# Kernel optimization log

Hardware: AMD Instinct MI355X
Metric: run time of the kernel (lower is better)

Reference implementation:

```python
import jax, jax.numpy as jnp
import numpy as np

TAU_PRE = 2.0
TAU_POST = 2.0
KH, KW = 3, 3
B, CIN, H, W = 16, 64, 66, 66
COUT = 128
HOUT, WOUT = H - KH + 1, W - KW + 1  # stride 1, padding 0


def setup_inputs() -> dict:
    key = jax.random.key(0)
    k1, k2, k3, k4, k5 = jax.random.split(key, 5)
    in_spike = jax.random.uniform(k1, (B, CIN, H, W), dtype=jnp.float32)
    out_spike = jax.random.uniform(k2, (B, COUT, HOUT, WOUT), dtype=jnp.float32)
    trace_pre = jax.random.uniform(k3, (B, CIN, H, W), dtype=jnp.float32)
    trace_post = jax.random.uniform(k4, (B, COUT, HOUT, WOUT), dtype=jnp.float32)
    weight = jax.random.normal(k5, (COUT, CIN, KH, KW), dtype=jnp.float32) * 0.05
    return {"in_spike": in_spike, "out_spike": out_spike,
            "trace_pre": trace_pre, "trace_post": trace_post, "weight": weight}


def reference(in_spike, out_spike, trace_pre, trace_post, weight):
    # Trace decay + spike accumulation (faithful to torch: tr - tr/tau + spike)
    tr_pre = trace_pre - trace_pre / TAU_PRE + in_spike    # [B,Cin,H,W]
    tr_post = trace_post - trace_post / TAU_POST + out_spike  # [B,Cout,Hout,Wout]

    rows = []
    for h in range(KH):
        cols = []
        for w in range(KW):
            pre = in_spike[:, :, h:h + HOUT, w:w + WOUT]   # [B,Cin,Hout,Wout]
            trp = tr_pre[:, :, h:h + HOUT, w:w + WOUT]     # [B,Cin,Hout,Wout]
            wk = weight[:, :, h, w]                        # [Cout,Cin]
            # sum over batch and spatial dims of outer products
            s_pre = jnp.einsum('bopq,bipq->oi', tr_post, pre)      # [Cout,Cin]
            s_post = jnp.einsum('bipq,bopq->oi', trp, out_spike)   # [Cout,Cin]
            cols.append(-wk * s_pre + wk * s_post)
        rows.append(jnp.stack(cols, axis=-1))  # [Cout,Cin,KW]
    delta_w = jnp.stack(rows, axis=-2)          # [Cout,Cin,KH,KW]
    return tr_pre, tr_post, delta_w
```

## Files before the change

### kernel.cpp

```cpp
#include <hip/hip_runtime.h>


typedef unsigned short ushort_t;
typedef unsigned int uint_t;
typedef __attribute__((ext_vector_type(8))) short short8;
typedef __attribute__((ext_vector_type(4))) float floatx4;
typedef __attribute__((ext_vector_type(2))) float floatx2;
typedef __attribute__((ext_vector_type(4))) int intx4;
typedef __attribute__((ext_vector_type(2))) unsigned int uintx2;

#define N_PRE   4460544
#define N_POST  8388608
#define N_DW    73728
#define O_TRPOST 4460544
#define O_DW     12849152
#define BROWS   67584
#define BRAW    4866048

#define FILL_A_BLOCKS 1280
#define FILL_B_BLOCKS 768
#define FILL_BLOCKS   2048
#define B_ROWS_PER_WAVE 22

#define GLDS16(g, l) __builtin_amdgcn_global_load_lds( \
    (const __attribute__((address_space(1))) void*)(g), \
    (__attribute__((address_space(3))) void*)(l), 16, 0, 0)

__device__ __forceinline__ ushort_t f2bf(float f) {
  uint_t u = __builtin_bit_cast(uint_t, f);
  u = (u + 0x7FFFu + ((u >> 16) & 1u)) >> 16;
  return (ushort_t)u;
}

__device__ __forceinline__ uint_t pk2bf(float a, float b) {
  return (uint_t)f2bf(a) | ((uint_t)f2bf(b) << 16);
}

__device__ __forceinline__ int bsh2(int hi, int lo) {
  return (int)((((unsigned long long)(uint_t)hi << 32) | (uint_t)lo) >> 16);
}

__global__ __launch_bounds__(256)
void k_fill(const float* __restrict__ in_sp, const float* __restrict__ out_sp,
            const float* __restrict__ tpre, const float* __restrict__ tpost,
            float* __restrict__ o_trpre, float* __restrict__ o_trpost,
            ushort_t* __restrict__ A1, ushort_t* __restrict__ A2,
            ushort_t* __restrict__ B1, ushort_t* __restrict__ B2, int use_ws) {
  const int bx = blockIdx.x;
  if (bx < FILL_A_BLOCKS) {
    const int n4 = N_POST / 4;
    const int stride = FILL_A_BLOCKS * 256;
    for (int i4 = bx * 256 + (int)threadIdx.x; i4 < n4; i4 += stride) {
      floatx4 o = *(const floatx4*)(out_sp + i4 * 4);
      floatx4 p = *(const floatx4*)(tpost + i4 * 4);
      *(floatx4*)(o_trpost + i4 * 4) = 0.5f * p + o;
      if (use_ws) {
        uintx2 va = { pk2bf(o.x, o.y), pk2bf(o.z, o.w) };
        uintx2 vn = { pk2bf(-p.x, -p.y), pk2bf(-p.z, -p.w) };
        *(uintx2*)(A1 + i4 * 4) = va;
        *(uintx2*)(A2 + i4 * 4) = vn;
      }
    }
  } else {
    const int l = threadIdx.x & 63;
    if (l >= 33) return;
    const int wid = (bx - FILL_A_BLOCKS) * 4 + ((int)threadIdx.x >> 6);
    #pragma unroll 2
    for (int it = 0; it < B_ROWS_PER_WAVE; ++it) {
      const int row = wid * B_ROWS_PER_WAVE + it;
      const int g = row * 66 + l * 2;
      floatx2 a = *(const floatx2*)(tpre + g);
      floatx2 c = *(const floatx2*)(in_sp + g);
      floatx2 v = { 0.5f * a.x + c.x, 0.5f * a.y + c.y };
      *(floatx2*)(o_trpre + g) = v;
      if (use_ws) {
        *(uint_t*)(B1 + row * 72 + l * 2) = pk2bf(a.x, a.y);
        *(uint_t*)(B2 + row * 72 + l * 2) = pk2bf(c.x, c.y);
      }
    }
  }
}

__global__ __launch_bounds__(256, 2)
void k_mfma(const ushort_t* __restrict__ A1, const ushort_t* __restrict__ B1,
            float* __restrict__ partials) {
  __shared__ short LA[16384];
  __shared__ short LB[64 * 152];

  const int kh = blockIdx.y, bx = blockIdx.x;
  const int b = bx >> 3, p0 = (bx & 7) * 8;
  const int t = threadIdx.x, w = t >> 6, l = t & 63;
  const int quad = l >> 4, l16 = l & 15;

  const int lr = l >> 4;
  const int gA = (l >> 3) & 1;
  const int mcE = (l & 7) ^ lr;
  const int matE = mcE >> 2, c4E = mcE & 3;
  const long aoffE = (long)matE * 8388608 + (long)(w & 1) * 262144
                   + lr * 4096 + gA * 32 + c4E * 8;
  const long aoffO = aoffE + (matE ? -8388608L : 8388608L);

  const int t2 = t & 127;

  floatx4 acc[3][2][4] = {};

  for (int rr = 0; rr < 8; ++rr) {
    const int p = p0 + rr, h = p + kh;
    __syncthreads();
    if (w < 2) {
      const ushort_t* ga = A1 + (long)b * 524288 + p * 64;
      #pragma unroll
      for (int j = 0; j < 16; ++j) {
        const ushort_t* src = ga + ((j & 1) ? aoffO : aoffE) + j * 16384;
        GLDS16(src, LA + (w & 1) * 8192 + j * 512);
      }
    } else {
      const ushort_t* gb = B1 + ((long)b * 4224 + h) * 72;
      #pragma unroll
      for (int k = 0; k < 9; ++k) {
        int c = k * 128 + t2;
        int i = c / 18, mc = c - i * 18;
        int mat = (mc >= 9) ? 1 : 0, ch9 = mc - mat * 9;
        intx4 v = *(const intx4*)(gb + (long)mat * BRAW + i * 4752 + ch9 * 8);
        *(intx4*)&LB[i * 152 + mat * 72 + ch9 * 8] = v;
      }
    }
    __syncthreads();

    #pragma unroll
    for (int ks = 0; ks < 2; ++ks) {
      short8 fa[2][2];
      #pragma unroll
      for (int mt = 0; mt < 2; ++mt) {
        const int o = w * 32 + mt * 16 + l16;
        #pragma unroll
        for (int mat = 0; mat < 2; ++mat)
          fa[mat][mt] = *(const short8*)&LA[o * 128 + ks * 64 + (((mat << 2) + quad) ^ (o & 7)) * 8];
      }
      #pragma unroll
      for (int nt = 0; nt < 4; ++nt) {
        const int i = nt * 16 + l16;
        short8 fb[2][3];
        #pragma unroll
        for (int mat = 0; mat < 2; ++mat) {
          const int base = i * 152 + mat * 72 + ks * 32 + quad * 8;
          intx4 W = *(const intx4*)&LB[base];
          int W4 = *(const int*)&LB[base + 8];
          intx4 f0 = { W.x, W.y, W.z, W.w };
          intx4 f1 = { bsh2(W.y, W.x), bsh2(W.z, W.y), bsh2(W.w, W.z), bsh2(W4, W.w) };
          intx4 f2 = { W.y, W.z, W.w, W4 };
          fb[mat][0] = __builtin_bit_cast(short8, f0);
          fb[mat][1] = __builtin_bit_cast(short8, f1);
          fb[mat][2] = __builtin_bit_cast(short8, f2);
        }
        #pragma unroll
        for (int kw = 0; kw < 3; ++kw)
          #pragma unroll
          for (int mt = 0; mt < 2; ++mt) {
            acc[kw][mt][nt] = __builtin_amdgcn_mfma_f32_16x16x32_bf16(fa[0][mt], fb[0][kw], acc[kw][mt][nt], 0, 0, 0);
            acc[kw][mt][nt] = __builtin_amdgcn_mfma_f32_16x16x32_bf16(fa[1][mt], fb[1][kw], acc[kw][mt][nt], 0, 0, 0);
          }
      }
    }
  }

  #pragma unroll
  for (int kw = 0; kw < 3; ++kw) {
    float* slice = partials + (size_t)((kh * 3 + kw) * 128 + bx) * 8192;
    #pragma unroll
    for (int mt = 0; mt < 2; ++mt)
      #pragma unroll
      for (int nt = 0; nt < 4; ++nt)
        #pragma unroll
        for (int rg = 0; rg < 4; ++rg) {
          const int o = w * 32 + mt * 16 + quad * 4 + rg;
          const int i = nt * 16 + l16;
          slice[o * 64 + i] = acc[kw][mt][nt][rg];
        }
  }
}

__global__ void k_finalize(const float* __restrict__ partials,
                           const float* __restrict__ weight, float* __restrict__ dw) {
  int tid = blockIdx.x * 256 + threadIdx.x;
  int e = tid >> 13, oi = tid & 8191;
  float s = 0.f;
  #pragma unroll 8
  for (int c = 0; c < 128; ++c) s += partials[(size_t)(e * 128 + c) * 8192 + oi];
  int o = oi >> 6, i = oi & 63;
  int wi = (o * 64 + i) * 9 + e;
  dw[wi] = 0.5f * weight[wi] * s;
}

__global__ void k_naive(const float* __restrict__ out_sp, const float* __restrict__ tpost,
                        const float* __restrict__ tpre, const float* __restrict__ in_sp,
                        const float* __restrict__ weight, float* __restrict__ dw) {
  int tid = blockIdx.x * 256 + threadIdx.x;
  int e = tid >> 13, oi = tid & 8191;
  int o = oi >> 6, i = oi & 63;
  int kh = e / 3, kw = e - kh * 3;
  float acc = 0.f;
  for (int b = 0; b < 16; ++b)
    for (int p = 0; p < 64; ++p) {
      const float* ga = out_sp + ((b * 128 + o) * 64 + p) * 64;
      const float* gn = tpost + ((b * 128 + o) * 64 + p) * 64;
      const float* gb = tpre + ((b * 64 + i) * 66 + p + kh) * 66 + kw;
      const float* gm = in_sp + ((b * 64 + i) * 66 + p + kh) * 66 + kw;
      for (int q = 0; q < 64; ++q) acc += ga[q] * gb[q] - gn[q] * gm[q];
    }
  int wi = (o * 64 + i) * 9 + kh * 3 + kw;
  dw[wi] = 0.5f * weight[wi] * acc;
}

extern "C" void kernel_launch(void* const* d_in, const int* in_sizes, int n_in,
                              void* d_out, int out_size, void* d_ws, size_t ws_size,
                              hipStream_t stream) {
  const float* in_sp  = (const float*)d_in[0];
  const float* out_sp = (const float*)d_in[1];
  const float* tpre   = (const float*)d_in[2];
  const float* tpost  = (const float*)d_in[3];
  const float* weight = (const float*)d_in[4];
  float* out = (float*)d_out;
  float* o_trpre  = out;
  float* o_trpost = out + O_TRPOST;
  float* o_dw     = out + O_DW;

  const size_t WS_NEED = 90767360;
  const int use_mfma = (ws_size >= WS_NEED) ? 1 : 0;
  ushort_t* A1 = (ushort_t*)d_ws;
  ushort_t* A2 = A1 + 8388608;
  ushort_t* B1 = A2 + 8388608;
  ushort_t* B2 = B1 + BRAW;
  float* partials = (float*)(B2 + BRAW);

  k_fill<<<FILL_BLOCKS, 256, 0, stream>>>(in_sp, out_sp, tpre, tpost,
                                          o_trpre, o_trpost, A1, A2, B1, B2, use_mfma);
  if (use_mfma) {
    dim3 g(128, 3);
    k_mfma<<<g, 256, 0, stream>>>(A1, B1, partials);
    k_finalize<<<N_DW / 256, 256, 0, stream>>>(partials, weight, o_dw);
  } else {
    k_naive<<<N_DW / 256, 256, 0, stream>>>(out_sp, tpost, tpre, in_sp, weight, o_dw);
  }
}
```

Baseline: 210.6 us.

## Fuse bf16 staging into MFMA kernel, converting fp32 inputs on the fly

Removes the bf16 workspace copies of the A and B operands. The MFMA blocks now read fp32 activations directly, convert them to bf16 with v_cvt_pk_bf16_f32, and keep A in registers while B is double-buffered in LDS. The trace-update fill and the MFMA work are merged into a single launch so the elementwise blocks and the GEMM blocks run concurrently. This cuts workspace write and read traffic and one kernel launch. In exchange, the MFMA blocks read fp32 instead of bf16 (more bytes per operand), the A loads come without LDS swizzle staging, and the MFMA blocks share the device with the bandwidth-heavy fill blocks.

```diff
diff --git a/kernel.cpp b/kernel.cpp
--- a/kernel.cpp
+++ b/kernel.cpp
@@ -7,135 +7,141 @@
 typedef __attribute__((ext_vector_type(4))) float floatx4;
 typedef __attribute__((ext_vector_type(2))) float floatx2;
 typedef __attribute__((ext_vector_type(4))) int intx4;
-typedef __attribute__((ext_vector_type(2))) unsigned int uintx2;
-
-#define N_PRE   4460544
-#define N_POST  8388608
-#define N_DW    73728
+typedef __attribute__((ext_vector_type(4))) uint_t uintx4;
+
+#define N_POST   8388608
+#define N_DW     73728
 #define O_TRPOST 4460544
 #define O_DW     12849152
-#define BROWS   67584
-#define BRAW    4866048
-
-#define FILL_A_BLOCKS 1280
-#define FILL_B_BLOCKS 768
-#define FILL_BLOCKS   2048
+
+#define MFMA_BLOCKS  384
+#define FILLA_BLOCKS 1024
+#define FILLB_BLOCKS 768
+#define TOTAL_BLOCKS 2176
 #define B_ROWS_PER_WAVE 22
 
-#define GLDS16(g, l) __builtin_amdgcn_global_load_lds( \
-    (const __attribute__((address_space(1))) void*)(g), \
-    (__attribute__((address_space(3))) void*)(l), 16, 0, 0)
-
-__device__ __forceinline__ ushort_t f2bf(float f) {
-  uint_t u = __builtin_bit_cast(uint_t, f);
-  u = (u + 0x7FFFu + ((u >> 16) & 1u)) >> 16;
-  return (ushort_t)u;
-}
-
-__device__ __forceinline__ uint_t pk2bf(float a, float b) {
-  return (uint_t)f2bf(a) | ((uint_t)f2bf(b) << 16);
-}
-
+__device__ __forceinline__ uint_t cvt2bf(float lo, float hi) {
+  uint_t r; asm("v_cvt_pk_bf16_f32 %0, %1, %2" : "=v"(r) : "v"(lo), "v"(hi)); return r;
+}
+__device__ __forceinline__ uint_t cvt2bfn(float lo, float hi) {
+  uint_t r; asm("v_cvt_pk_bf16_f32 %0, -%1, -%2" : "=v"(r) : "v"(lo), "v"(hi)); return r;
+}
 __device__ __forceinline__ int bsh2(int hi, int lo) {
   return (int)((((unsigned long long)(uint_t)hi << 32) | (uint_t)lo) >> 16);
 }
 
-__global__ __launch_bounds__(256)
-void k_fill(const float* __restrict__ in_sp, const float* __restrict__ out_sp,
+__global__ __launch_bounds__(256, 2)
+void k_main(const float* __restrict__ in_sp, const float* __restrict__ out_sp,
             const float* __restrict__ tpre, const float* __restrict__ tpost,
             float* __restrict__ o_trpre, float* __restrict__ o_trpost,
-            ushort_t* __restrict__ A1, ushort_t* __restrict__ A2,
-            ushort_t* __restrict__ B1, ushort_t* __restrict__ B2, int use_ws) {
-  const int bx = blockIdx.x;
-  if (bx < FILL_A_BLOCKS) {
-    const int n4 = N_POST / 4;
-    const int stride = FILL_A_BLOCKS * 256;
-    for (int i4 = bx * 256 + (int)threadIdx.x; i4 < n4; i4 += stride) {
-      floatx4 o = *(const floatx4*)(out_sp + i4 * 4);
-      floatx4 p = *(const floatx4*)(tpost + i4 * 4);
-      *(floatx4*)(o_trpost + i4 * 4) = 0.5f * p + o;
-      if (use_ws) {
-        uintx2 va = { pk2bf(o.x, o.y), pk2bf(o.z, o.w) };
-        uintx2 vn = { pk2bf(-p.x, -p.y), pk2bf(-p.z, -p.w) };
-        *(uintx2*)(A1 + i4 * 4) = va;
-        *(uintx2*)(A2 + i4 * 4) = vn;
-      }
-    }
-  } else {
-    const int l = threadIdx.x & 63;
-    if (l >= 33) return;
-    const int wid = (bx - FILL_A_BLOCKS) * 4 + ((int)threadIdx.x >> 6);
-    #pragma unroll 2
-    for (int it = 0; it < B_ROWS_PER_WAVE; ++it) {
-      const int row = wid * B_ROWS_PER_WAVE + it;
-      const int g = row * 66 + l * 2;
-      floatx2 a = *(const floatx2*)(tpre + g);
-      floatx2 c = *(const floatx2*)(in_sp + g);
-      floatx2 v = { 0.5f * a.x + c.x, 0.5f * a.y + c.y };
-      *(floatx2*)(o_trpre + g) = v;
-      if (use_ws) {
-        *(uint_t*)(B1 + row * 72 + l * 2) = pk2bf(a.x, a.y);
-        *(uint_t*)(B2 + row * 72 + l * 2) = pk2bf(c.x, c.y);
-      }
-    }
-  }
-}
-
-__global__ __launch_bounds__(256, 2)
-void k_mfma(const ushort_t* __restrict__ A1, const ushort_t* __restrict__ B1,
-            float* __restrict__ partials) {
-  __shared__ short LA[16384];
-  __shared__ short LB[64 * 152];
-
-  const int kh = blockIdx.y, bx = blockIdx.x;
+            float* __restrict__ partials, int use_ws) {
+  const int bx0 = blockIdx.x;
+  const int t = threadIdx.x;
+
+  if (bx0 >= MFMA_BLOCKS) {
+    if (bx0 < MFMA_BLOCKS + FILLA_BLOCKS) {
+      int i4 = (bx0 - MFMA_BLOCKS) * 256 + t;
+      #pragma unroll
+      for (int it = 0; it < 8; ++it, i4 += FILLA_BLOCKS * 256) {
+        floatx4 o = *(const floatx4*)(out_sp + i4 * 4);
+        floatx4 p = *(const floatx4*)(tpost + i4 * 4);
+        *(floatx4*)(o_trpost + i4 * 4) = 0.5f * p + o;
+      }
+    } else {
+      const int l = t & 63;
+      if (l >= 33) return;
+      const int wid = (bx0 - (MFMA_BLOCKS + FILLA_BLOCKS)) * 4 + (t >> 6);
+      #pragma unroll 2
+      for (int it = 0; it < B_ROWS_PER_WAVE; ++it) {
+        const int g = (wid * B_ROWS_PER_WAVE + it) * 66 + l * 2;
+        floatx2 a = *(const floatx2*)(tpre + g);
+        floatx2 c = *(const floatx2*)(in_sp + g);
+        floatx2 v = { 0.5f * a.x + c.x, 0.5f * a.y + c.y };
+        *(floatx2*)(o_trpre + g) = v;
+      }
+    }
+    return;
+  }
+  if (!use_ws) return;
+
+  __shared__ short LB[2][9728];
+  const int kh = bx0 >> 7, bx = bx0 & 127;
   const int b = bx >> 3, p0 = (bx & 7) * 8;
-  const int t = threadIdx.x, w = t >> 6, l = t & 63;
+  const int w = t >> 6, l = t & 63;
   const int quad = l >> 4, l16 = l & 15;
-
-  const int lr = l >> 4;
-  const int gA = (l >> 3) & 1;
-  const int mcE = (l & 7) ^ lr;
-  const int matE = mcE >> 2, c4E = mcE & 3;
-  const long aoffE = (long)matE * 8388608 + (long)(w & 1) * 262144
-                   + lr * 4096 + gA * 32 + c4E * 8;
-  const long aoffO = aoffE + (matE ? -8388608L : 8388608L);
-
-  const int t2 = t & 127;
+  const int si = t >> 2, sg = t & 3;
+
+  const float* arow0 = out_sp + ((b * 128 + w * 32 + l16) * 4096 + quad * 8 + p0 * 64);
+  const float* arow1 = tpost  + ((b * 128 + w * 32 + l16) * 4096 + quad * 8 + p0 * 64);
+  const float* brow0 = tpre  + ((b * 64 + si) * 66 * 66 + sg * 16);
+  const float* brow1 = in_sp + ((b * 64 + si) * 66 * 66 + sg * 16);
+  short* Lrow = &LB[0][0] + si * 152 + sg * 16;
 
   floatx4 acc[3][2][4] = {};
 
+  auto stageB = [&](int h, int buf) {
+    const float* r0 = brow0 + h * 66;
+    const float* r1 = brow1 + h * 66;
+    floatx2 v0[8], v1[8];
+    #pragma unroll
+    for (int k = 0; k < 8; ++k) {
+      v0[k] = *(const floatx2*)(r0 + 2 * k);
+      v1[k] = *(const floatx2*)(r1 + 2 * k);
+    }
+    uintx4 u0a = { cvt2bf(v0[0].x, v0[0].y), cvt2bf(v0[1].x, v0[1].y),
+                   cvt2bf(v0[2].x, v0[2].y), cvt2bf(v0[3].x, v0[3].y) };
+    uintx4 u0b = { cvt2bf(v0[4].x, v0[4].y), cvt2bf(v0[5].x, v0[5].y),
+                   cvt2bf(v0[6].x, v0[6].y), cvt2bf(v0[7].x, v0[7].y) };
+    uintx4 u1a = { cvt2bf(v1[0].x, v1[0].y), cvt2bf(v1[1].x, v1[1].y),
+                   cvt2bf(v1[2].x, v1[2].y), cvt2bf(v1[3].x, v1[3].y) };
+    uintx4 u1b = { cvt2bf(v1[4].x, v1[4].y), cvt2bf(v1[5].x, v1[5].y),
+                   cvt2bf(v1[6].x, v1[6].y), cvt2bf(v1[7].x, v1[7].y) };
+    short* Lb = Lrow + buf * 9728;
+    *(uintx4*)(Lb)      = u0a;
+    *(uintx4*)(Lb + 8)  = u0b;
+    *(uintx4*)(Lb + 72) = u1a;
+    *(uintx4*)(Lb + 80) = u1b;
+    if (sg == 3) {
+      floatx2 t0 = *(const floatx2*)(r0 + 16);
+      floatx2 t1 = *(const floatx2*)(r1 + 16);
+      *(uint_t*)(Lb + 16) = cvt2bf(t0.x, t0.y);
+      *(uint_t*)(Lb + 88) = cvt2bf(t1.x, t1.y);
+    }
+  };
+
+  stageB(p0 + kh, 0);
+  __syncthreads();
+
   for (int rr = 0; rr < 8; ++rr) {
-    const int p = p0 + rr, h = p + kh;
-    __syncthreads();
-    if (w < 2) {
-      const ushort_t* ga = A1 + (long)b * 524288 + p * 64;
-      #pragma unroll
-      for (int j = 0; j < 16; ++j) {
-        const ushort_t* src = ga + ((j & 1) ? aoffO : aoffE) + j * 16384;
-        GLDS16(src, LA + (w & 1) * 8192 + j * 512);
-      }
-    } else {
-      const ushort_t* gb = B1 + ((long)b * 4224 + h) * 72;
-      #pragma unroll
-      for (int k = 0; k < 9; ++k) {
-        int c = k * 128 + t2;
-        int i = c / 18, mc = c - i * 18;
-        int mat = (mc >= 9) ? 1 : 0, ch9 = mc - mat * 9;
-        intx4 v = *(const intx4*)(gb + (long)mat * BRAW + i * 4752 + ch9 * 8);
-        *(intx4*)&LB[i * 152 + mat * 72 + ch9 * 8] = v;
-      }
-    }
-    __syncthreads();
-
+    floatx4 ar[2][2][2][2];
+    #pragma unroll
+    for (int mt = 0; mt < 2; ++mt)
+      #pragma unroll
+      for (int ks = 0; ks < 2; ++ks)
+        #pragma unroll
+        for (int hf = 0; hf < 2; ++hf) {
+          const int off = rr * 64 + mt * 65536 + ks * 32 + hf * 4;
+          ar[0][mt][ks][hf] = *(const floatx4*)(arow0 + off);
+          ar[1][mt][ks][hf] = *(const floatx4*)(arow1 + off);
+        }
+    if (rr < 7) stageB(p0 + rr + 1 + kh, (rr + 1) & 1);
+
+    const short* Lbb = &LB[0][0] + (rr & 1) * 9728;
     #pragma unroll
     for (int ks = 0; ks < 2; ++ks) {
       short8 fa[2][2];
       #pragma unroll
       for (int mt = 0; mt < 2; ++mt) {
-        const int o = w * 32 + mt * 16 + l16;
-        #pragma unroll
-        for (int mat = 0; mat < 2; ++mat)
-          fa[mat][mt] = *(const short8*)&LA[o * 128 + ks * 64 + (((mat << 2) + quad) ^ (o & 7)) * 8];
+        uintx4 ua = { cvt2bf (ar[0][mt][ks][0].x, ar[0][mt][ks][0].y),
+                      cvt2bf (ar[0][mt][ks][0].z, ar[0][mt][ks][0].w),
+                      cvt2bf (ar[0][mt][ks][1].x, ar[0][mt][ks][1].y),
+                      cvt2bf (ar[0][mt][ks][1].z, ar[0][mt][ks][1].w) };
+        uintx4 un = { cvt2bfn(ar[1][mt][ks][0].x, ar[1][mt][ks][0].y),
+                      cvt2bfn(ar[1][mt][ks][0].z, ar[1][mt][ks][0].w),
+                      cvt2bfn(ar[1][mt][ks][1].x, ar[1][mt][ks][1].y),
+                      cvt2bfn(ar[1][mt][ks][1].z, ar[1][mt][ks][1].w) };
+        fa[0][mt] = __builtin_bit_cast(short8, ua);
+        fa[1][mt] = __builtin_bit_cast(short8, un);
       }
       #pragma unroll
       for (int nt = 0; nt < 4; ++nt) {
@@ -144,8 +150,8 @@
         #pragma unroll
         for (int mat = 0; mat < 2; ++mat) {
           const int base = i * 152 + mat * 72 + ks * 32 + quad * 8;
-          intx4 W = *(const intx4*)&LB[base];
-          int W4 = *(const int*)&LB[base + 8];
+          intx4 W = *(const intx4*)&Lbb[base];
+          int W4 = *(const int*)&Lbb[base + 8];
           intx4 f0 = { W.x, W.y, W.z, W.w };
           intx4 f1 = { bsh2(W.y, W.x), bsh2(W.z, W.y), bsh2(W.w, W.z), bsh2(W4, W.w) };
           intx4 f2 = { W.y, W.z, W.w, W4 };
@@ -162,6 +168,7 @@
           }
       }
     }
+    __syncthreads();
   }
 
   #pragma unroll
@@ -225,19 +232,13 @@
   float* o_trpost = out + O_TRPOST;
   float* o_dw     = out + O_DW;
 
-  const size_t WS_NEED = 90767360;
+  const size_t WS_NEED = (size_t)9 * 128 * 8192 * 4;
   const int use_mfma = (ws_size >= WS_NEED) ? 1 : 0;
-  ushort_t* A1 = (ushort_t*)d_ws;
-  ushort_t* A2 = A1 + 8388608;
-  ushort_t* B1 = A2 + 8388608;
-  ushort_t* B2 = B1 + BRAW;
-  float* partials = (float*)(B2 + BRAW);
-
-  k_fill<<<FILL_BLOCKS, 256, 0, stream>>>(in_sp, out_sp, tpre, tpost,
-                                          o_trpre, o_trpost, A1, A2, B1, B2, use_mfma);
+  float* partials = (float*)d_ws;
+
+  k_main<<<TOTAL_BLOCKS, 256, 0, stream>>>(in_sp, out_sp, tpre, tpost,
+                                           o_trpre, o_trpost, partials, use_mfma);
   if (use_mfma) {
-    dim3 g(128, 3);
-    k_mfma<<<g, 256, 0, stream>>>(A1, B1, partials);
     k_finalize<<<N_DW / 256, 256, 0, stream>>>(partials, weight, o_dw);
   } else {
     k_naive<<<N_DW / 256, 256, 0, stream>>>(out_sp, tpost, tpre, in_sp, weight, o_dw);
```

After: 198.2 us (median of 2 runs). -5.9%, faster.
